# Kernel optimization log

Measured on AMD Instinct MI355X. Metric: run time of the kernel, lower is better.

The kernel has to match this reference:

```python
import jax, jax.numpy as jnp
import numpy as np

N = 100000
E = 3200000
IN_DIM = 512
HID = 256
NUM_CLASSES = 16
P_DROP = 0.5
EPS_BN = 1e-5


def setup_inputs() -> dict:
    key = jax.random.key(0)
    ks = jax.random.split(key, 6)
    x = jax.random.normal(ks[0], (N, IN_DIM), jnp.float32)
    edge_src = jax.random.randint(ks[1], (E,), 0, N, dtype=jnp.int32)
    edge_dst = jax.random.randint(ks[2], (E,), 0, N, dtype=jnp.int32)
    # Glorot-ish init for GraphConv weights (bias=False in the module)
    W1 = jax.random.normal(ks[3], (IN_DIM, HID), jnp.float32) / np.sqrt(IN_DIM).astype(np.float32)
    W2 = jax.random.normal(ks[4], (HID, NUM_CLASSES), jnp.float32) / np.sqrt(HID).astype(np.float32)
    W3 = jax.random.normal(ks[5], (HID, NUM_CLASSES), jnp.float32) / np.sqrt(HID).astype(np.float32)
    return {"x": x, "W1": W1, "W2": W2, "W3": W3,
            "edge_src": edge_src, "edge_dst": edge_dst}


def _graph_conv(h, W, edge_src, edge_dst, out_inv_sqrt, in_inv_sqrt):
    # DGL GraphConv, norm='both', bias=False:
    #   rst = D_in^{-1/2} * A_agg( D_out^{-1/2} * h @ W )
    # Apply W before aggregation (out_dim <= in_dim here); same math as DGL.
    h = h * out_inv_sqrt[:, None]          # [N, d_in]
    h = h @ W                              # [N, d_out]
    agg = jax.ops.segment_sum(h[edge_src], edge_dst, num_segments=h.shape[0])
    return agg * in_inv_sqrt[:, None]


def _dropout(key, x, p=P_DROP):
    keep = jax.random.bernoulli(key, 1.0 - p, x.shape)
    return jnp.where(keep, x / (1.0 - p), jnp.zeros((), x.dtype))


def reference(x, W1, W2, W3, edge_src, edge_dst):
    n = x.shape[0]
    ones = jnp.ones(edge_src.shape[0], x.dtype)
    out_deg = jax.ops.segment_sum(ones, edge_src, num_segments=n)
    in_deg = jax.ops.segment_sum(ones, edge_dst, num_segments=n)
    out_is = jnp.maximum(out_deg, 1.0) ** -0.5   # DGL clamps degree to min 1
    in_is = jnp.maximum(in_deg, 1.0) ** -0.5

    k1, k2a, k2b, keps = jax.random.split(jax.random.key(42), 4)

    # gc1 + relu
    h = _dropout(k1, x)
    h = jax.nn.relu(_graph_conv(h, W1, edge_src, edge_dst, out_is, in_is))

    # BatchNorm1d(affine=False, track_running_stats=False): batch stats
    mean = jnp.mean(h, axis=0)
    var = jnp.var(h, axis=0)
    h = (h - mean) * jax.lax.rsqrt(var + EPS_BN)

    # gc2 (mu) and gc3 (logvar), each with its own dropout of hidden1
    mu = _graph_conv(_dropout(k2a, h), W2, edge_src, edge_dst, out_is, in_is)
    logvar = _graph_conv(_dropout(k2b, h), W3, edge_src, edge_dst, out_is, in_is)

    # reparameterize (training): eps * exp(logvar) + mu  (note: exp(logvar), per source)
    eps = jax.random.normal(keps, mu.shape, mu.dtype)
    return eps * jnp.exp(logvar) + mu
```

## Files before the change

### kernel.cpp

```cpp
#include <hip/hip_runtime.h>
#include <stdint.h>

#define N_NODES 100000
#define N_EDGES 3200000
#define IN_DIM  512
#define HID     256
#define NCLS    16

#define DBLK   256
#define DCHUNK (N_EDGES / DBLK)
#define DWIN2  50000
#define NBKT   98
#define NTILE  ((N_NODES + 255) / 256)

typedef unsigned short u16;
typedef __attribute__((ext_vector_type(8))) short short8;
typedef __attribute__((ext_vector_type(4))) float float4v;

__device__ __forceinline__ float bf2f(u16 u) {
  return __uint_as_float(((uint32_t)u) << 16);
}
__device__ __forceinline__ u16 f2bf(float f) {
  uint32_t u = __float_as_uint(f);
  return (u16)((u + 0x7fffu + ((u >> 16) & 1u)) >> 16);
}
__device__ __forceinline__ void acc8(float* a, uint4 v) {
  a[0] += bf2f((u16)(v.x & 0xffffu)); a[1] += bf2f((u16)(v.x >> 16));
  a[2] += bf2f((u16)(v.y & 0xffffu)); a[3] += bf2f((u16)(v.y >> 16));
  a[4] += bf2f((u16)(v.z & 0xffffu)); a[5] += bf2f((u16)(v.z >> 16));
  a[6] += bf2f((u16)(v.w & 0xffffu)); a[7] += bf2f((u16)(v.w >> 16));
}

__device__ __forceinline__ void gload16(const void* g, void* l) {
  __builtin_amdgcn_global_load_lds(
      (const __attribute__((address_space(1))) uint32_t*)g,
      (__attribute__((address_space(3))) uint32_t*)l, 16, 0, 0);
}

__host__ __device__ __forceinline__ uint32_t rotl32(uint32_t v, int d) {
  return (v << d) | (v >> (32 - d));
}

__host__ __device__ __forceinline__ void threefry2x32(uint32_t k0, uint32_t k1,
    uint32_t x0, uint32_t x1, uint32_t& o0, uint32_t& o1) {
  uint32_t ks0 = k0, ks1 = k1, ks2 = k0 ^ k1 ^ 0x1BD11BDAu;
  x0 += ks0; x1 += ks1;
#define TF_R(r) { x0 += x1; x1 = rotl32(x1, r); x1 ^= x0; }
  TF_R(13) TF_R(15) TF_R(26) TF_R(6)
  x0 += ks1; x1 += ks2 + 1u;
  TF_R(17) TF_R(29) TF_R(16) TF_R(24)
  x0 += ks2; x1 += ks0 + 2u;
  TF_R(13) TF_R(15) TF_R(26) TF_R(6)
  x0 += ks0; x1 += ks1 + 3u;
  TF_R(17) TF_R(29) TF_R(16) TF_R(24)
  x0 += ks1; x1 += ks2 + 4u;
  TF_R(13) TF_R(15) TF_R(26) TF_R(6)
  x0 += ks2; x1 += ks0 + 5u;
#undef TF_R
  o0 = x0; o1 = x1;
}

__host__ __device__ __forceinline__ uint32_t tf_bits32(uint32_t k0, uint32_t k1, uint32_t idx) {
  uint32_t o0, o1;
  threefry2x32(k0, k1, 0u, idx, o0, o1);
  return o0 ^ o1;
}

__device__ __forceinline__ float erfinv_f32(float x) {
  float w = -log1pf(-x * x);
  float p;
  if (w < 5.0f) {
    w -= 2.5f;
    p = 2.81022636e-08f;
    p = fmaf(p, w, 3.43273939e-07f);
    p = fmaf(p, w, -3.5233877e-06f);
    p = fmaf(p, w, -4.39150654e-06f);
    p = fmaf(p, w, 0.00021858087f);
    p = fmaf(p, w, -0.00125372503f);
    p = fmaf(p, w, -0.00417768164f);
    p = fmaf(p, w, 0.246640727f);
    p = fmaf(p, w, 1.50140941f);
  } else {
    w = sqrtf(w) - 3.0f;
    p = -0.000200214257f;
    p = fmaf(p, w, 0.000100950558f);
    p = fmaf(p, w, 0.00134934322f);
    p = fmaf(p, w, -0.00367342844f);
    p = fmaf(p, w, 0.00573950773f);
    p = fmaf(p, w, -0.0076224613f);
    p = fmaf(p, w, 0.00943887047f);
    p = fmaf(p, w, 1.00167406f);
    p = fmaf(p, w, 2.83297682f);
  }
  return p * x;
}

__global__ __launch_bounds__(1024) void hist_part_k(
    const int* __restrict__ esrc, const int* __restrict__ edst,
    u16* __restrict__ P16, uint32_t* __restrict__ bofs_g,
    unsigned long long* __restrict__ ebuf) {
  __shared__ uint32_t h32[DWIN2 / 2];
  __shared__ uint32_t bcnt[NBKT + 1];
  const int b = blockIdx.x, tid = threadIdx.x;
  const int ebase = b * DCHUNK;
  if (tid < NBKT + 1) bcnt[tid] = 0u;
  for (int w = 0; w < 2; ++w) {
    const int lo = w * DWIN2;
    for (int i = tid; i < DWIN2 / 2; i += 1024) h32[i] = 0u;
    __syncthreads();
    for (int e = ebase + tid; e < ebase + DCHUNK; e += 1024) {
      int s = esrc[e], d = edst[e];
      unsigned su = (unsigned)(s - lo);
      if (su < (unsigned)DWIN2) atomicAdd(&h32[su >> 1], 1u << ((su & 1) * 16));
      unsigned du = (unsigned)(d - lo);
      if (du < (unsigned)DWIN2) atomicAdd(&h32[du >> 1], 0x100u << ((du & 1) * 16));
      if (w == 0) atomicAdd(&bcnt[d >> 10], 1u);
    }
    __syncthreads();
    for (int i = tid; i < DWIN2 / 2; i += 1024) {
      *(uint32_t*)(P16 + (size_t)b * N_NODES + lo + 2 * i) = h32[i];
    }
    __syncthreads();
  }
  if (tid == 0) {
    uint32_t run = 0;
    for (int k = 0; k < NBKT; ++k) { uint32_t c = bcnt[k]; bcnt[k] = run; run += c; }
    bcnt[NBKT] = run;
  }
  __syncthreads();
  if (tid < NBKT + 1) bofs_g[b * (NBKT + 1) + tid] = bcnt[tid];
  __syncthreads();
  for (int e = ebase + tid; e < ebase + DCHUNK; e += 1024) {
    int d = edst[e], s = esrc[e];
    uint32_t slot = atomicAdd(&bcnt[d >> 10], 1u);
    ebuf[(size_t)b * DCHUNK + slot] = ((unsigned long long)(uint32_t)s << 32) | (uint32_t)d;
  }
}

__global__ void degsum_k(const u16* __restrict__ P16, float* __restrict__ out_is,
                         float* __restrict__ in_is, int* __restrict__ row_ofs,
                         int* __restrict__ tile_sum) {
  const int tid = threadIdx.x;
  const int n = blockIdx.x * 256 + tid;
  const int lane = tid & 63, wv = tid >> 6;
  uint32_t to = 0, ti = 0;
  if (n < N_NODES) {
#pragma unroll 8
    for (int b = 0; b < DBLK; ++b) {
      uint32_t v = P16[(size_t)b * N_NODES + n];
      to += v & 0xffu; ti += v >> 8;
    }
    out_is[n] = rsqrtf(fmaxf((float)to, 1.0f));
    in_is[n]  = rsqrtf(fmaxf((float)ti, 1.0f));
  }
  int sc = (int)ti;
#pragma unroll
  for (int d = 1; d < 64; d <<= 1) {
    int t = __shfl_up(sc, d, 64);
    if (lane >= d) sc += t;
  }
  __shared__ int ws[4];
  if (lane == 63) ws[wv] = sc;
  __syncthreads();
  int wbase = 0;
#pragma unroll
  for (int i = 0; i < 4; ++i) if (i < wv) wbase += ws[i];
  if (n < N_NODES) row_ofs[n] = wbase + sc - (int)ti;
  if (tid == 0) tile_sum[blockIdx.x] = ws[0] + ws[1] + ws[2] + ws[3];
}

__global__ void fixup_k(const int* __restrict__ tile_sum, int* __restrict__ row_ofs) {
  const int b = blockIdx.x, tid = threadIdx.x;
  const int lane = tid & 63, wv = tid >> 6;
  int v = 0;
  if (tid < b) v = tile_sum[tid];
  if (tid + 256 < b) v += tile_sum[tid + 256];
#pragma unroll
  for (int m = 1; m < 64; m <<= 1) v += __shfl_xor(v, m, 64);
  __shared__ int wr[4];
  if (lane == 0) wr[wv] = v;
  __syncthreads();
  const int base = wr[0] + wr[1] + wr[2] + wr[3];
  const int n = b * 256 + tid;
  if (n < N_NODES) row_ofs[n] += base;
  if (b == (int)gridDim.x - 1 && tid == 0) row_ofs[N_NODES] = base + tile_sum[b];
}

__global__ __launch_bounds__(1024) void bplace_k(
    const unsigned long long* __restrict__ ebuf, const uint32_t* __restrict__ bofs_g,
    const int* __restrict__ row_ofs, int* __restrict__ csr) {
  __shared__ uint32_t cur[1024];
  const int k = blockIdx.x, tid = threadIdx.x;
  const int lane = tid & 63, wv = tid >> 6;
  const int dbase = k << 10;
  int nd = N_NODES - dbase; if (nd > 1024) nd = 1024;
  if (tid < nd) cur[tid] = (uint32_t)row_ofs[dbase + tid];
  __syncthreads();
  for (int b = wv; b < DBLK; b += 16) {
    uint32_t st = bofs_g[b * (NBKT + 1) + k];
    uint32_t en = bofs_g[b * (NBKT + 1) + k + 1];
    for (uint32_t i = st + lane; i < en; i += 64) {
      unsigned long long v = ebuf[(size_t)b * DCHUNK + i];
      int d = (int)(uint32_t)(v & 0xffffffffu);
      int s = (int)(uint32_t)(v >> 32);
      uint32_t slot = atomicAdd(&cur[d - dbase], 1u);
      csr[slot] = s;
    }
  }
}

__global__ void cast_w_k(const float* __restrict__ W1, const float* __restrict__ W2,
                         const float* __restrict__ W3, u16* __restrict__ W1t,
                         u16* __restrict__ Wt23) {
  int idx = blockIdx.x * blockDim.x + threadIdx.x;
  if (idx < IN_DIM * HID) {
    int k = idx >> 8, n = idx & 255;
    W1t[n * IN_DIM + k] = f2bf(W1[idx]);
  } else {
    int t = idx - IN_DIM * HID;
    int n = t >> 8, k = t & 255;
    float v = (n < 16) ? W2[k * NCLS + n] : W3[k * NCLS + (n - 16)];
    Wt23[n * HID + k] = f2bf(v);
  }
}

#define G1_BM 128
#define G1_BKC 8
__global__ __launch_bounds__(512, 2) void gemm1_k(
    const float* __restrict__ x, const float* __restrict__ out_is,
    uint32_t k0, uint32_t k1,
    const u16* __restrict__ W1t, u16* __restrict__ X1b) {
  __shared__ u16 As[G1_BM * 64];
  __shared__ u16 Bs[256 * 64];
  const int tid = threadIdx.x;
  const int wid = tid >> 6, lane = tid & 63;
  const int wr = wid >> 2, wc = wid & 3;
  const int m16 = lane & 15, q = lane >> 4;
  const int srow = lane >> 3, schunk = lane & 7;
  const long base_row = (long)blockIdx.x * G1_BM;

  const int arow_l = tid >> 2, acp = tid & 3;
  const long agrow = base_row + arow_l;
  const long asrow = (agrow < N_NODES) ? agrow : (N_NODES - 1);
  const float asc = 2.0f * out_is[asrow];
  const float* xrow = x + asrow * IN_DIM;
  const int aw0 = ((2 * acp)     ^ (arow_l & 7)) * 8;
  const int aw1 = ((2 * acp + 1) ^ (arow_l & 7)) * 8;

  float4v acc[4][4];
#pragma unroll
  for (int i = 0; i < 4; ++i)
#pragma unroll
    for (int j = 0; j < 4; ++j) acc[i][j] = (float4v)0.0f;

  for (int ks = 0; ks < IN_DIM / 64; ++ks) {
    const int kbase = ks * 64 + acp * 16;
    float4 f0 = *(const float4*)(xrow + kbase);
    float4 f1 = *(const float4*)(xrow + kbase + 4);
    float4 f2 = *(const float4*)(xrow + kbase + 8);
    float4 f3 = *(const float4*)(xrow + kbase + 12);
    float xv[16] = {f0.x, f0.y, f0.z, f0.w, f1.x, f1.y, f1.z, f1.w,
                    f2.x, f2.y, f2.z, f2.w, f3.x, f3.y, f3.z, f3.w};
    const uint32_t ibase = (uint32_t)asrow * IN_DIM + (uint32_t)kbase;
    u16 ob[16];
#pragma unroll
    for (int j = 0; j < 16; ++j) {
      uint32_t bits = tf_bits32(k0, k1, ibase + (uint32_t)j);
      ob[j] = f2bf((bits >> 31) ? 0.0f : xv[j] * asc);
    }
    uint4 pka, pkb;
    pka.x = (uint32_t)ob[0] | ((uint32_t)ob[1] << 16);
    pka.y = (uint32_t)ob[2] | ((uint32_t)ob[3] << 16);
    pka.z = (uint32_t)ob[4] | ((uint32_t)ob[5] << 16);
    pka.w = (uint32_t)ob[6] | ((uint32_t)ob[7] << 16);
    pkb.x = (uint32_t)ob[8] | ((uint32_t)ob[9] << 16);
    pkb.y = (uint32_t)ob[10] | ((uint32_t)ob[11] << 16);
    pkb.z = (uint32_t)ob[12] | ((uint32_t)ob[13] << 16);
    pkb.w = (uint32_t)ob[14] | ((uint32_t)ob[15] << 16);
    *(uint4*)(As + arow_l * 64 + aw0) = pka;
    *(uint4*)(As + arow_l * 64 + aw1) = pkb;
#pragma unroll
    for (int i = 0; i < 4; ++i) {
      int j = wid * 4 + i;
      int n = j * 8 + srow;
      int gch = ks * G1_BKC + (schunk ^ (n & 7));
      gload16(W1t + (size_t)n * IN_DIM + gch * 8, Bs + j * 512);
    }
    __syncthreads();
#pragma unroll
    for (int kk = 0; kk < 2; ++kk) {
      short8 a[4], b[4];
      const int kq = kk * 4 + q;
      const int c = kq ^ (m16 & 7);
#pragma unroll
      for (int rt = 0; rt < 4; ++rt) {
        int row = wr * 64 + rt * 16 + m16;
        a[rt] = *(const short8*)(As + row * 64 + c * 8);
      }
#pragma unroll
      for (int ct = 0; ct < 4; ++ct) {
        int n = wc * 64 + ct * 16 + m16;
        b[ct] = *(const short8*)(Bs + n * 64 + c * 8);
      }
#pragma unroll
      for (int rt = 0; rt < 4; ++rt)
#pragma unroll
        for (int ct = 0; ct < 4; ++ct)
          acc[rt][ct] = __builtin_amdgcn_mfma_f32_16x16x32_bf16(a[rt], b[ct], acc[rt][ct], 0, 0, 0);
    }
    __syncthreads();
  }
#pragma unroll
  for (int rt = 0; rt < 4; ++rt) {
#pragma unroll
    for (int r = 0; r < 4; ++r) {
      long grow = base_row + wr * 64 + rt * 16 + q * 4 + r;
      if (grow < N_NODES) {
#pragma unroll
        for (int ct = 0; ct < 4; ++ct)
          X1b[grow * HID + wc * 64 + ct * 16 + m16] = f2bf(acc[rt][ct][r]);
      }
    }
  }
}

__global__ __launch_bounds__(256) void agg_relu_k(
    const u16* __restrict__ X1b, const int* __restrict__ row_ofs,
    const int* __restrict__ csr, const float* __restrict__ in_is,
    u16* __restrict__ h1b) {
  int d = blockIdx.x * 4 + (threadIdx.x >> 6);
  int lane = threadIdx.x & 63;
  int half = lane >> 5;
  int col = (lane & 31) * 8;
  int beg = row_ofs[d], end = row_ofs[d + 1];
  float a[8];
#pragma unroll
  for (int i = 0; i < 8; ++i) a[i] = 0.0f;
  int j = beg + half;
  for (; j + 14 < end; j += 16) {
    int s0 = csr[j],      s1 = csr[j + 2],  s2 = csr[j + 4],  s3 = csr[j + 6];
    int s4 = csr[j + 8],  s5 = csr[j + 10], s6 = csr[j + 12], s7 = csr[j + 14];
    uint4 v0 = *(const uint4*)(X1b + (size_t)s0 * HID + col);
    uint4 v1 = *(const uint4*)(X1b + (size_t)s1 * HID + col);
    uint4 v2 = *(const uint4*)(X1b + (size_t)s2 * HID + col);
    uint4 v3 = *(const uint4*)(X1b + (size_t)s3 * HID + col);
    uint4 v4 = *(const uint4*)(X1b + (size_t)s4 * HID + col);
    uint4 v5 = *(const uint4*)(X1b + (size_t)s5 * HID + col);
    uint4 v6 = *(const uint4*)(X1b + (size_t)s6 * HID + col);
    uint4 v7 = *(const uint4*)(X1b + (size_t)s7 * HID + col);
    acc8(a, v0); acc8(a, v1); acc8(a, v2); acc8(a, v3);
    acc8(a, v4); acc8(a, v5); acc8(a, v6); acc8(a, v7);
  }
  for (; j + 6 < end; j += 8) {
    int s0 = csr[j], s1 = csr[j + 2], s2 = csr[j + 4], s3 = csr[j + 6];
    uint4 v0 = *(const uint4*)(X1b + (size_t)s0 * HID + col);
    uint4 v1 = *(const uint4*)(X1b + (size_t)s1 * HID + col);
    uint4 v2 = *(const uint4*)(X1b + (size_t)s2 * HID + col);
    uint4 v3 = *(const uint4*)(X1b + (size_t)s3 * HID + col);
    acc8(a, v0); acc8(a, v1); acc8(a, v2); acc8(a, v3);
  }
  for (; j < end; j += 2) {
    uint4 v0 = *(const uint4*)(X1b + (size_t)csr[j] * HID + col);
    acc8(a, v0);
  }
#pragma unroll
  for (int i = 0; i < 8; ++i) a[i] += __shfl(a[i], lane ^ 32, 64);
  if (half == 0) {
    float is = in_is[d];
    u16 o[8];
#pragma unroll
    for (int i = 0; i < 8; ++i) o[i] = f2bf(fmaxf(a[i] * is, 0.0f));
    uint4 pk;
    pk.x = (uint32_t)o[0] | ((uint32_t)o[1] << 16);
    pk.y = (uint32_t)o[2] | ((uint32_t)o[3] << 16);
    pk.z = (uint32_t)o[4] | ((uint32_t)o[5] << 16);
    pk.w = (uint32_t)o[6] | ((uint32_t)o[7] << 16);
    *(uint4*)(h1b + (size_t)d * HID + col) = pk;
  }
}

__global__ __launch_bounds__(256) void bn_stats_k(const u16* __restrict__ h1b,
                                                  float* __restrict__ bn) {
  __shared__ float ls[512];
  const int tid = threadIdx.x;
  const int cb = (tid & 31) * 8;
  const int ms = tid >> 5;
  float s[8], s2[8];
#pragma unroll
  for (int i = 0; i < 8; ++i) { s[i] = 0.f; s2[i] = 0.f; }
  for (int m = ms;; m += 8) {
    int r = blockIdx.x + 256 * m;
    if (r >= N_NODES) break;
    uint4 v = *(const uint4*)(h1b + (size_t)r * HID + cb);
    float f[8];
    f[0] = bf2f((u16)(v.x & 0xffffu)); f[1] = bf2f((u16)(v.x >> 16));
    f[2] = bf2f((u16)(v.y & 0xffffu)); f[3] = bf2f((u16)(v.y >> 16));
    f[4] = bf2f((u16)(v.z & 0xffffu)); f[5] = bf2f((u16)(v.z >> 16));
    f[6] = bf2f((u16)(v.w & 0xffffu)); f[7] = bf2f((u16)(v.w >> 16));
#pragma unroll
    for (int i = 0; i < 8; ++i) { s[i] += f[i]; s2[i] += f[i] * f[i]; }
  }
  ls[tid] = 0.f; ls[tid + 256] = 0.f;
  __syncthreads();
#pragma unroll
  for (int i = 0; i < 8; ++i) {
    atomicAdd(&ls[cb + i], s[i]);
    atomicAdd(&ls[256 + cb + i], s2[i]);
  }
  __syncthreads();
  atomicAdd(&bn[tid], ls[tid]);
  atomicAdd(&bn[HID + tid], ls[256 + tid]);
}

#define WLS 264
__global__ __launch_bounds__(256) void gemm23_k(
    const u16* __restrict__ h1b, const u16* __restrict__ Wt23,
    uint32_t ka0, uint32_t ka1, uint32_t kb0, uint32_t kb1,
    const float* __restrict__ out_is, const float* __restrict__ bn,
    u16* __restrict__ XMLV) {
  __shared__ u16 Wls[32 * WLS];
  __shared__ float cB[HID], cA[HID];
  const int tid = threadIdx.x;
#pragma unroll
  for (int i = 0; i < 4; ++i) {
    int idx = tid + i * 256;
    int n = idx >> 5, c = idx & 31;
    *(uint4*)(Wls + n * WLS + c * 8) = ((const uint4*)Wt23)[idx];
  }
  {
    float mean = bn[tid] * (1.0f / (float)N_NODES);
    float var = bn[HID + tid] * (1.0f / (float)N_NODES) - mean * mean;
    float istd = rsqrtf(var + 1e-5f);
    cB[tid] = istd;
    cA[tid] = -mean * istd;
  }
  __syncthreads();

  const int wv = tid >> 6, lane = tid & 63;
  const int m = lane & 15, q = lane >> 4;
  const long arow = (long)blockIdx.x * 64 + wv * 16 + m;
  const bool valid = arow < N_NODES;
  const float osc = valid ? 2.0f * out_is[arow] : 0.0f;
  const uint32_t rbase = (uint32_t)(valid ? arow : 0) * HID;

  float4v accM = (float4v)0.0f, accL = (float4v)0.0f;
  for (int kc = 0; kc < HID; kc += 32) {
    const int kof = kc + q * 8;
    uint4 hv = make_uint4(0, 0, 0, 0);
    if (valid) hv = *(const uint4*)(h1b + arow * HID + kof);
    float4 B0 = *(const float4*)(cB + kof);
    float4 B1 = *(const float4*)(cB + kof + 4);
    float4 A0 = *(const float4*)(cA + kof);
    float4 A1 = *(const float4*)(cA + kof + 4);
    float hval[8] = {
      bf2f((u16)(hv.x & 0xffffu)), bf2f((u16)(hv.x >> 16)),
      bf2f((u16)(hv.y & 0xffffu)), bf2f((u16)(hv.y >> 16)),
      bf2f((u16)(hv.z & 0xffffu)), bf2f((u16)(hv.z >> 16)),
      bf2f((u16)(hv.w & 0xffffu)), bf2f((u16)(hv.w >> 16))};
    float nb[8] = {B0.x, B0.y, B0.z, B0.w, B1.x, B1.y, B1.z, B1.w};
    float na[8] = {A0.x, A0.y, A0.z, A0.w, A1.x, A1.y, A1.z, A1.w};
    const uint32_t ibase = rbase + (uint32_t)kof;
    short8 Aa, Ab;
#pragma unroll
    for (int jj = 0; jj < 8; ++jj) {
      float t = fmaf(hval[jj], nb[jj], na[jj]) * osc;
      u16 tb = f2bf(t);
      uint32_t ba = tf_bits32(ka0, ka1, ibase + (uint32_t)jj);
      uint32_t bb = tf_bits32(kb0, kb1, ibase + (uint32_t)jj);
      Aa[jj] = (short)((ba >> 31) ? 0 : tb);
      Ab[jj] = (short)((bb >> 31) ? 0 : tb);
    }
    short8 Bm = *(const short8*)(Wls + m * WLS + kof);
    short8 Bl = *(const short8*)(Wls + (16 + m) * WLS + kof);
    accM = __builtin_amdgcn_mfma_f32_16x16x32_bf16(Aa, Bm, accM, 0, 0, 0);
    accL = __builtin_amdgcn_mfma_f32_16x16x32_bf16(Ab, Bl, accL, 0, 0, 0);
  }
#pragma unroll
  for (int r = 0; r < 4; ++r) {
    long srow = (long)blockIdx.x * 64 + wv * 16 + q * 4 + r;
    if (srow < N_NODES) {
      XMLV[srow * 32 + m]      = f2bf(accM[r]);
      XMLV[srow * 32 + 16 + m] = f2bf(accL[r]);
    }
  }
}

__global__ __launch_bounds__(256) void agg_final_k(
    const u16* __restrict__ XMLV, const int* __restrict__ row_ofs,
    const int* __restrict__ csr, const float* __restrict__ in_is,
    uint32_t ke0, uint32_t ke1, float* __restrict__ out) {
  int g = blockIdx.x * 4 + (threadIdx.x >> 6);
  int lane = threadIdx.x & 63;
  int half = lane >> 5, c = lane & 31;
  int beg = row_ofs[g], end = row_ofs[g + 1];
  float s = 0.f;
  int j = beg + half;
  for (; j + 14 < end; j += 16) {
    int s0 = csr[j],      s1 = csr[j + 2],  s2 = csr[j + 4],  s3 = csr[j + 6];
    int s4 = csr[j + 8],  s5 = csr[j + 10], s6 = csr[j + 12], s7 = csr[j + 14];
    float v0 = bf2f(XMLV[(size_t)s0 * 32 + c]);
    float v1 = bf2f(XMLV[(size_t)s1 * 32 + c]);
    float v2 = bf2f(XMLV[(size_t)s2 * 32 + c]);
    float v3 = bf2f(XMLV[(size_t)s3 * 32 + c]);
    float v4 = bf2f(XMLV[(size_t)s4 * 32 + c]);
    float v5 = bf2f(XMLV[(size_t)s5 * 32 + c]);
    float v6 = bf2f(XMLV[(size_t)s6 * 32 + c]);
    float v7 = bf2f(XMLV[(size_t)s7 * 32 + c]);
    s += v0; s += v1; s += v2; s += v3;
    s += v4; s += v5; s += v6; s += v7;
  }
#pragma unroll
  for (int k = 0; k < 8; ++k) {
    int e = j + 2 * k;
    if (e < end) s += bf2f(XMLV[(size_t)csr[e] * 32 + c]);
  }
  s += __shfl(s, lane ^ 32, 64);
  if (half == 0) {
    s *= in_is[g];
    float other = __shfl(s, lane ^ 16, 64);
    if (c < 16) {
      uint32_t i = (uint32_t)(g * NCLS + c);
      uint32_t bits = tf_bits32(ke0, ke1, i);
      float f = __uint_as_float((bits >> 9) | 0x3f800000u) - 1.0f;
      const float lo = -0.99999994f;
      float u = fmaxf(lo, fmaf(f, 2.0f, lo));
      float eps = 1.41421356f * erfinv_f32(u);
      out[i] = eps * expf(other) + s;
    }
  }
}

extern "C" void kernel_launch(void* const* d_in, const int* in_sizes, int n_in,
                              void* d_out, int out_size, void* d_ws, size_t ws_size,
                              hipStream_t stream) {
  (void)in_sizes; (void)n_in; (void)out_size; (void)ws_size;
  const float* x  = (const float*)d_in[0];
  const float* W1 = (const float*)d_in[1];
  const float* W2 = (const float*)d_in[2];
  const float* W3 = (const float*)d_in[3];
  const int* esrc = (const int*)d_in[4];
  const int* edst = (const int*)d_in[5];
  float* out = (float*)d_out;

  uint32_t kb[8];
  for (int j = 0; j < 4; ++j)
    threefry2x32(0u, 42u, 0u, (uint32_t)j, kb[2 * j], kb[2 * j + 1]);

  char* p = (char*)d_ws;
  auto take = [&](size_t bytes) -> void* {
    void* r = (void*)p;
    p += (bytes + 255) & ~(size_t)255;
    return r;
  };
  u16* P16       = (u16*)take(sizeof(u16) * (size_t)DBLK * N_NODES);
  unsigned long long* ebuf = (unsigned long long*)take(sizeof(unsigned long long) * (size_t)N_EDGES);
  u16* X1b       = (u16*)take(sizeof(u16) * (size_t)N_NODES * HID);
  u16* h1b       = (u16*)take(sizeof(u16) * (size_t)N_NODES * HID);
  u16* XMLV      = (u16*)take(sizeof(u16) * (size_t)N_NODES * 32);
  u16* W1t       = (u16*)take(sizeof(u16) * (size_t)IN_DIM * HID);
  u16* Wt23      = (u16*)take(sizeof(u16) * 32 * HID);
  uint32_t* bofs_g = (uint32_t*)take(sizeof(uint32_t) * (size_t)DBLK * (NBKT + 1));
  int* tile_sum  = (int*)take(sizeof(int) * NTILE);
  float* out_is  = (float*)take(sizeof(float) * N_NODES);
  float* in_is   = (float*)take(sizeof(float) * N_NODES);
  int* row_ofs   = (int*)take(sizeof(int) * (N_NODES + 1));
  int* csr       = (int*)take(sizeof(int) * N_EDGES);
  float* bn      = (float*)take(sizeof(float) * 1024);

  hipMemsetAsync(bn, 0, sizeof(float) * 512, stream);

  hist_part_k<<<DBLK, 1024, 0, stream>>>(esrc, edst, P16, bofs_g, ebuf);
  degsum_k<<<NTILE, 256, 0, stream>>>(P16, out_is, in_is, row_ofs, tile_sum);
  fixup_k<<<NTILE, 256, 0, stream>>>(tile_sum, row_ofs);
  bplace_k<<<NBKT, 1024, 0, stream>>>(ebuf, bofs_g, row_ofs, csr);

  cast_w_k<<<(IN_DIM * HID + 32 * HID) / 256, 256, 0, stream>>>(W1, W2, W3, W1t, Wt23);

  gemm1_k<<<(N_NODES + G1_BM - 1) / G1_BM, 512, 0, stream>>>(x, out_is, kb[0], kb[1], W1t, X1b);
  agg_relu_k<<<N_NODES / 4, 256, 0, stream>>>(X1b, row_ofs, csr, in_is, h1b);
  bn_stats_k<<<256, 256, 0, stream>>>(h1b, bn);
  gemm23_k<<<(N_NODES + 63) / 64, 256, 0, stream>>>(h1b, Wt23, kb[2], kb[3], kb[4], kb[5],
                                                    out_is, bn, XMLV);
  agg_final_k<<<N_NODES / 4, 256, 0, stream>>>(XMLV, row_ofs, csr, in_is, kb[6], kb[7], out);
}
```

Baseline: 908.8 us.

## Precompute dropout bitmasks for gc2/gc3 inside the memory-bound aggregation kernel

The Threefry dropout-bit generation for the two hidden-layer dropouts moves out of gemm23_k and into agg_relu_k. There, each thread builds one byte of packed keep bits and writes it to the mska/mskb buffers. The idea is to hide the ALU-heavy RNG under the gather-bound aggregation, so gemm23_k only loads a 32-bit mask word per chunk. This adds about 6.4MB of mask writes and reads. It relies on the aggregation grid having exactly enough threads to cover both masks (N*HID/8*2 == N/4*256).

Measured after the change: 841.3 us. 1.08x faster.

```diff
diff --git a/kernel.cpp b/kernel.cpp
--- a/kernel.cpp
+++ b/kernel.cpp
@@ -14,6 +14,7 @@
 #define NTILE  ((N_NODES + 255) / 256)
 
 typedef unsigned short u16;
+typedef unsigned char u8;
 typedef __attribute__((ext_vector_type(8))) short short8;
 typedef __attribute__((ext_vector_type(4))) float float4v;
 
@@ -327,6 +328,8 @@
 __global__ __launch_bounds__(256) void agg_relu_k(
     const u16* __restrict__ X1b, const int* __restrict__ row_ofs,
     const int* __restrict__ csr, const float* __restrict__ in_is,
+    uint32_t ka0, uint32_t ka1, uint32_t kb0, uint32_t kb1,
+    u8* __restrict__ mska, u8* __restrict__ mskb,
     u16* __restrict__ h1b) {
   int d = blockIdx.x * 4 + (threadIdx.x >> 6);
   int lane = threadIdx.x & 63;
@@ -377,6 +380,19 @@
     pk.w = (uint32_t)o[6] | ((uint32_t)o[7] << 16);
     *(uint4*)(h1b + (size_t)d * HID + col) = pk;
   }
+  {
+    const uint32_t NB = (uint32_t)N_NODES * HID / 8;
+    uint32_t gid = blockIdx.x * 256u + threadIdx.x;
+    const bool isB = gid >= NB;
+    const uint32_t mi = isB ? gid - NB : gid;
+    const uint32_t kk0 = isB ? kb0 : ka0, kk1 = isB ? kb1 : ka1;
+    const uint32_t ib = mi * 8u;
+    uint32_t bits = 0u;
+#pragma unroll
+    for (uint32_t jj = 0; jj < 8; ++jj)
+      bits |= ((~tf_bits32(kk0, kk1, ib + jj)) >> 31) << jj;
+    (isB ? mskb : mska)[mi] = (u8)bits;
+  }
 }
 
 __global__ __launch_bounds__(256) void bn_stats_k(const u16* __restrict__ h1b,
@@ -415,7 +431,7 @@
 #define WLS 264
 __global__ __launch_bounds__(256) void gemm23_k(
     const u16* __restrict__ h1b, const u16* __restrict__ Wt23,
-    uint32_t ka0, uint32_t ka1, uint32_t kb0, uint32_t kb1,
+    const u8* __restrict__ mska, const u8* __restrict__ mskb,
     const float* __restrict__ out_is, const float* __restrict__ bn,
     u16* __restrict__ XMLV) {
   __shared__ u16 Wls[32 * WLS];
@@ -441,13 +457,18 @@
   const long arow = (long)blockIdx.x * 64 + wv * 16 + m;
   const bool valid = arow < N_NODES;
   const float osc = valid ? 2.0f * out_is[arow] : 0.0f;
-  const uint32_t rbase = (uint32_t)(valid ? arow : 0) * HID;
 
   float4v accM = (float4v)0.0f, accL = (float4v)0.0f;
   for (int kc = 0; kc < HID; kc += 32) {
     const int kof = kc + q * 8;
     uint4 hv = make_uint4(0, 0, 0, 0);
-    if (valid) hv = *(const uint4*)(h1b + arow * HID + kof);
+    uint32_t wa = 0, wb = 0;
+    if (valid) {
+      hv = *(const uint4*)(h1b + arow * HID + kof);
+      uint32_t bofs = ((uint32_t)arow * HID + (uint32_t)kc) >> 3;
+      wa = (*(const uint32_t*)(mska + bofs)) >> (q * 8);
+      wb = (*(const uint32_t*)(mskb + bofs)) >> (q * 8);
+    }
     float4 B0 = *(const float4*)(cB + kof);
     float4 B1 = *(const float4*)(cB + kof + 4);
     float4 A0 = *(const float4*)(cA + kof);
@@ -459,16 +480,13 @@
       bf2f((u16)(hv.w & 0xffffu)), bf2f((u16)(hv.w >> 16))};
     float nb[8] = {B0.x, B0.y, B0.z, B0.w, B1.x, B1.y, B1.z, B1.w};
     float na[8] = {A0.x, A0.y, A0.z, A0.w, A1.x, A1.y, A1.z, A1.w};
-    const uint32_t ibase = rbase + (uint32_t)kof;
     short8 Aa, Ab;
 #pragma unroll
     for (int jj = 0; jj < 8; ++jj) {
       float t = fmaf(hval[jj], nb[jj], na[jj]) * osc;
       u16 tb = f2bf(t);
-      uint32_t ba = tf_bits32(ka0, ka1, ibase + (uint32_t)jj);
-      uint32_t bb = tf_bits32(kb0, kb1, ibase + (uint32_t)jj);
-      Aa[jj] = (short)((ba >> 31) ? 0 : tb);
-      Ab[jj] = (short)((bb >> 31) ? 0 : tb);
+      Aa[jj] = (short)(((wa >> jj) & 1u) ? tb : 0);
+      Ab[jj] = (short)(((wb >> jj) & 1u) ? tb : 0);
     }
     short8 Bm = *(const short8*)(Wls + m * WLS + kof);
     short8 Bl = *(const short8*)(Wls + (16 + m) * WLS + kof);
@@ -559,6 +577,8 @@
   u16* XMLV      = (u16*)take(sizeof(u16) * (size_t)N_NODES * 32);
   u16* W1t       = (u16*)take(sizeof(u16) * (size_t)IN_DIM * HID);
   u16* Wt23      = (u16*)take(sizeof(u16) * 32 * HID);
+  u8* mska       = (u8*)take((size_t)N_NODES * HID / 8);
+  u8* mskb       = (u8*)take((size_t)N_NODES * HID / 8);
   uint32_t* bofs_g = (uint32_t*)take(sizeof(uint32_t) * (size_t)DBLK * (NBKT + 1));
   int* tile_sum  = (int*)take(sizeof(int) * NTILE);
   float* out_is  = (float*)take(sizeof(float) * N_NODES);
@@ -577,9 +597,9 @@
   cast_w_k<<<(IN_DIM * HID + 32 * HID) / 256, 256, 0, stream>>>(W1, W2, W3, W1t, Wt23);
 
   gemm1_k<<<(N_NODES + G1_BM - 1) / G1_BM, 512, 0, stream>>>(x, out_is, kb[0], kb[1], W1t, X1b);
-  agg_relu_k<<<N_NODES / 4, 256, 0, stream>>>(X1b, row_ofs, csr, in_is, h1b);
+  agg_relu_k<<<N_NODES / 4, 256, 0, stream>>>(X1b, row_ofs, csr, in_is,
+                                              kb[2], kb[3], kb[4], kb[5], mska, mskb, h1b);
   bn_stats_k<<<256, 256, 0, stream>>>(h1b, bn);
-  gemm23_k<<<(N_NODES + 63) / 64, 256, 0, stream>>>(h1b, Wt23, kb[2], kb[3], kb[4], kb[5],
-                                                    out_is, bn, XMLV);
+  gemm23_k<<<(N_NODES + 63) / 64, 256, 0, stream>>>(h1b, Wt23, mska, mskb, out_is, bn, XMLV);
   agg_final_k<<<N_NODES / 4, 256, 0, stream>>>(XMLV, row_ofs, csr, in_is, kb[6], kb[7], out);
 }
```
